# Kernel tuning notes

Hardware: AMD Instinct MI355X
Metric: run time of the kernel (lower is better)

The kernel has to match this reference:

```python
import jax, jax.numpy as jnp
import numpy as np

N = 100000      # nodes
E = 1600000     # edges
IN, H1, H2, OUT = 128, 128, 64, 128  # layer_channel = [128, (128+128)//2, (128+128)//4, 128]


def setup_inputs() -> dict:
    key = jax.random.key(0)
    ks = jax.random.split(key, 11)
    w = lambda k, s: (jax.random.normal(k, s, jnp.float32) * 0.05)
    return {
        "x": jax.random.normal(ks[0], (N, IN), jnp.float32),
        "edge_index": jax.random.randint(ks[1], (2, E), 0, N),
        "gcn1_w": w(ks[2], (IN, H1)),   "gcn1_b": jnp.zeros((H1,), jnp.float32),
        "fc2_w": w(ks[3], (H1, H1)),   # nn.Linear weight [out, in]
        "gcn3_w": w(ks[4], (H1, H2)),   "gcn3_b": jnp.zeros((H2,), jnp.float32),
        "fc4_w": w(ks[5], (H2, H2)),
        "gcn5_w": w(ks[6], (H2, OUT)),  "gcn5_b": jnp.zeros((OUT,), jnp.float32),
        "fc6_w": w(ks[7], (OUT, OUT)),
    }


def _gcn_norm(edge_index):
    # PyG GCNConv default: add self-loops, symmetric normalization D^-1/2 (A+I) D^-1/2
    loop = jnp.arange(N, dtype=edge_index.dtype)
    src = jnp.concatenate([edge_index[0], loop])
    dst = jnp.concatenate([edge_index[1], loop])
    deg = jax.ops.segment_sum(jnp.ones_like(src, jnp.float32), dst, num_segments=N)
    dinv = jnp.where(deg > 0, jax.lax.rsqrt(jnp.maximum(deg, 1.0)), 0.0)
    norm = dinv[src] * dinv[dst]  # [E+N]
    return src, dst, norm


def _gcn_conv(x, W, b, src, dst, norm):
    h = x @ W                              # [N, d_out]
    msg = h[src] * norm[:, None]           # gather + scale over edges
    return jax.ops.segment_sum(msg, dst, num_segments=N) + b


def reference(x, edge_index, gcn1_w, gcn1_b, fc2_w, gcn3_w, gcn3_b, fc4_w, gcn5_w, gcn5_b, fc6_w):
    src, dst, norm = _gcn_norm(edge_index)
    relu = jax.nn.relu
    z1 = relu(_gcn_conv(x, gcn1_w, gcn1_b, src, dst, norm))
    z1 = relu(z1 + z1 @ fc2_w.T)
    z2 = relu(_gcn_conv(z1, gcn3_w, gcn3_b, src, dst, norm))
    z2 = relu(z2 + z2 @ fc4_w.T)
    z3 = relu(_gcn_conv(z2, gcn5_w, gcn5_b, src, dst, norm))
    z3 = relu(z3 + z3 @ fc6_w.T)
    return z3
```

## Files before the change

### kernel.cpp

```cpp
#include <hip/hip_runtime.h>
#include <cstdint>
#include <cstddef>

#define NN 100000
#define NE 1600000
#define NBB 391
#define BSTRIDE 5120

typedef short short8 __attribute__((ext_vector_type(8)));
typedef float floatx4 __attribute__((ext_vector_type(4)));
typedef unsigned short u16;
typedef uint32_t u32;


static __global__ void k_zero(int* __restrict__ gcur) {
    int i = threadIdx.x;
    if (i < NBB + 1) gcur[i] = 0;
}

static __global__ __launch_bounds__(1024) void k_bscatterF(const int* __restrict__ src,
                                                           const int* __restrict__ dst,
                                                           int* __restrict__ gcur,
                                                           int2* __restrict__ staging) {
    __shared__ int h[NBB + 1];
    __shared__ int base[NBB + 1];
    int t = threadIdx.x;
    for (int i = t; i < NBB; i += 1024) h[i] = 0;
    __syncthreads();
    int e0 = blockIdx.x * 4096;
    int b[4], l[4], sv[4], dv[4];
#pragma unroll
    for (int j = 0; j < 4; j++) {
        int e = e0 + j * 1024 + t;
        b[j] = -1;
        if (e < NE) {
            sv[j] = src[e];
            dv[j] = dst[e];
            b[j] = dv[j] >> 8;
            l[j] = atomicAdd(&h[b[j]], 1);
        }
    }
    __syncthreads();
    for (int i = t; i < NBB; i += 1024)
        if (h[i]) base[i] = atomicAdd(&gcur[i], h[i]);
    __syncthreads();
#pragma unroll
    for (int j = 0; j < 4; j++)
        if (b[j] >= 0)
            staging[(size_t)b[j] * BSTRIDE + base[b[j]] + l[j]] = make_int2(sv[j], dv[j]);
}

static __global__ __launch_bounds__(1024) void k_blocal2(const int2* __restrict__ staging,
                                                         const int* __restrict__ gcur,
                                                         float* __restrict__ dinv,
                                                         int* __restrict__ row_ptr) {
    __shared__ int cnt[256];
    __shared__ int sc[256];
    int b = blockIdx.x;
    int t = threadIdx.x;
    if (t < 256) cnt[t] = 0;
    __syncthreads();
    const int n = gcur[b];
    const int base = b * BSTRIDE;
    for (int i = base + t; i < base + n; i += 1024)
        atomicAdd(&cnt[staging[i].y & 255], 1);
    __syncthreads();
    int myc = (t < 256) ? cnt[t] : 0;
    if (t < 256) sc[t] = myc;
    __syncthreads();
    for (int off = 1; off < 256; off <<= 1) {
        int x = 0;
        if (t < 256 && t >= off) x = sc[t - off];
        __syncthreads();
        if (t < 256) sc[t] += x;
        __syncthreads();
    }
    if (t < 256) {
        int node = (b << 8) + t;
        if (node < NN) {
            dinv[node] = rsqrtf((float)(myc + 1));
            row_ptr[node] = sc[t] - myc;
        }
    }
}

static __global__ void k_bscanB(const int* __restrict__ gcur, int* __restrict__ gbase,
                                int* __restrict__ row_ptr) {
    __shared__ int sd[512];
    int t = threadIdx.x;
    int v = (t < NBB) ? gcur[t] : 0;
    sd[t] = v;
    __syncthreads();
    for (int off = 1; off < 512; off <<= 1) {
        int x = (t >= off) ? sd[t - off] : 0;
        __syncthreads();
        sd[t] += x;
        __syncthreads();
    }
    int excl = (t > 0) ? sd[t - 1] : 0;
    if (t < NBB) gbase[t] = excl;
    if (t == NBB) gbase[NBB] = excl;
    if (t == 0) row_ptr[NN] = NE;
}

static __global__ __launch_bounds__(1024) void k_bfill2(const int2* __restrict__ staging,
                                                        const int* __restrict__ gcur,
                                                        const int* __restrict__ gbase,
                                                        int* __restrict__ row_ptr,
                                                        int* __restrict__ csr_src) {
    __shared__ int cnt[256];
    __shared__ int lrp[256];
    int b = blockIdx.x;
    int t = threadIdx.x;
    if (t < 256) {
        cnt[t] = 0;
        int node = (b << 8) + t;
        lrp[t] = (node < NN) ? row_ptr[node] : 0;
    }
    __syncthreads();
    const int bb = gbase[b];
    const int n = gcur[b];
    const int base = b * BSTRIDE;
    for (int i = base + t; i < base + n; i += 1024) {
        int2 ed = staging[i];
        int loc = ed.y & 255;
        int r = atomicAdd(&cnt[loc], 1);
        csr_src[bb + lrp[loc] + r] = ed.x;
    }
    if (t < 256) {
        int node = (b << 8) + t;
        if (node < NN) row_ptr[node] = bb + lrp[t];
    }
}

__device__ __forceinline__ void split_bf16(float f, short& hi, short& lo) {
    union { float f; uint32_t u; } x;
    x.f = f;
    uint32_t uh = x.u + 0x7FFFu + ((x.u >> 16) & 1u);
    hi = (short)(uh >> 16);
    union { uint32_t u; float f; } hf;
    hf.u = (uh >> 16) << 16;
    float r = f - hf.f;
    union { float f; uint32_t u; } y;
    y.f = r;
    uint32_t ul = y.u + 0x7FFFu + ((y.u >> 16) & 1u);
    lo = (short)(ul >> 16);
}

__device__ __forceinline__ u16 f2bf(float f) {
    union { float f; uint32_t u; } x;
    x.f = f;
    uint32_t r = x.u + 0x7FFFu + ((x.u >> 16) & 1u);
    return (u16)(r >> 16);
}

__device__ __forceinline__ float bf2f(u16 h) {
    union { uint32_t u; float f; } x;
    x.u = ((uint32_t)h) << 16;
    return x.f;
}

__device__ __forceinline__ void acc2(uint32_t u, float& a0, float& a1) {
    union { uint32_t u; float f; } lo, hi;
    lo.u = u << 16;
    hi.u = u & 0xFFFF0000u;
    a0 += lo.f;
    a1 += hi.f;
}

struct WDesc {
    const float* W;
    short* fh;
    short* fl;
    int din, dout, transb, base, total;
};
struct WPrepArgs { WDesc d[6]; };

static __global__ void k_wprep(WPrepArgs args) {
    int tid = blockIdx.x * 256 + threadIdx.x;
#pragma unroll
    for (int i = 0; i < 6; i++) {
        const WDesc& D = args.d[i];
        if (tid >= D.base && tid < D.base + D.total) {
            int local = tid - D.base;
            int lane = local & 63;
            int rest = local >> 6;
            int kst = D.din >> 5;
            int ks = rest % kst;
            int ntile = rest / kst;
            int n = ntile * 16 + (lane & 15);
            int k0 = ks * 32 + (lane >> 4) * 8;
#pragma unroll
            for (int j = 0; j < 8; j++) {
                int k = k0 + j;
                float v = D.transb ? D.W[(size_t)n * D.din + k]
                                   : D.W[(size_t)k * D.dout + n];
                short h, l;
                split_bf16(v, h, l);
                D.fh[(size_t)local * 8 + j] = h;
                D.fl[(size_t)local * 8 + j] = l;
            }
        }
    }
}

template <int DIN, int DOUT, int MT, int AMODE, int OMODE, bool RESID, bool BIAS, bool SCALE>
__global__ __launch_bounds__(256, 3) void k_mgemm(const void* __restrict__ Av,
                                                  const short* __restrict__ fh,
                                                  const short* __restrict__ fl,
                                                  const float* __restrict__ bias,
                                                  const float* __restrict__ dinv,
                                                  void* __restrict__ C) {
    static_assert(!RESID || DIN == DOUT, "residual needs square");
    constexpr int KST = DIN / 32;
    constexpr int NTW = DOUT / 64;
    const int t = threadIdx.x;
    const int wave = t >> 6;
    const int lane = t & 63;
    const int r16 = lane & 15;
    const int kq = lane >> 4;

    const float* Af = (const float*)Av;
    const u16*   Ah = (const u16*)Av;
    const u16*   Al = Ah + (size_t)NN * DIN;

    short8 bh[NTW][KST], bl[NTW][KST];
#pragma unroll
    for (int nt = 0; nt < NTW; nt++) {
        int ntile = wave * NTW + nt;
#pragma unroll
        for (int ks = 0; ks < KST; ks++) {
            size_t o = ((size_t)(ntile * KST + ks) * 64 + lane) * 8;
            bh[nt][ks] = *(const short8*)(fh + o);
            bl[nt][ks] = *(const short8*)(fl + o);
        }
    }

    const int m0b = blockIdx.x * (MT * 16);
#pragma unroll
    for (int mt = 0; mt < MT; mt++) {
        const int m0 = m0b + mt * 16;
        if (m0 >= NN) break;
        const int ra = min(m0 + r16, NN - 1);

        floatx4 acc[NTW];
#pragma unroll
        for (int nt = 0; nt < NTW; nt++) acc[nt] = (floatx4){0.f, 0.f, 0.f, 0.f};

        if constexpr (AMODE == 1) {
            const float* Ap = Af + (size_t)ra * DIN + kq * 8;
#pragma unroll
            for (int ks = 0; ks < KST; ks++) {
                float4 f0 = *(const float4*)(Ap + ks * 32);
                float4 f1 = *(const float4*)(Ap + ks * 32 + 4);
                float fe[8] = {f0.x, f0.y, f0.z, f0.w, f1.x, f1.y, f1.z, f1.w};
                short8 ah;
#pragma unroll
                for (int j = 0; j < 8; j++) ah[j] = (short)f2bf(fe[j]);
#pragma unroll
                for (int nt = 0; nt < NTW; nt++) {
                    acc[nt] = __builtin_amdgcn_mfma_f32_16x16x32_bf16(ah, bh[nt][ks], acc[nt], 0, 0, 0);
                    acc[nt] = __builtin_amdgcn_mfma_f32_16x16x32_bf16(ah, bl[nt][ks], acc[nt], 0, 0, 0);
                }
            }
        } else {
            const u16* Aph = Ah + (size_t)ra * DIN + kq * 8;
            const u16* Apl = Al + (size_t)ra * DIN + kq * 8;
#pragma unroll
            for (int ks = 0; ks < KST; ks++) {
                short8 ah = *(const short8*)(Aph + ks * 32);
                short8 al = *(const short8*)(Apl + ks * 32);
#pragma unroll
                for (int nt = 0; nt < NTW; nt++) {
                    acc[nt] = __builtin_amdgcn_mfma_f32_16x16x32_bf16(ah, bh[nt][ks], acc[nt], 0, 0, 0);
                    acc[nt] = __builtin_amdgcn_mfma_f32_16x16x32_bf16(ah, bl[nt][ks], acc[nt], 0, 0, 0);
                    acc[nt] = __builtin_amdgcn_mfma_f32_16x16x32_bf16(al, bh[nt][ks], acc[nt], 0, 0, 0);
                }
            }
        }

#pragma unroll
        for (int nt = 0; nt < NTW; nt++) {
            int col = (wave * NTW + nt) * 16 + r16;
#pragma unroll
            for (int r = 0; r < 4; r++) {
                int row = m0 + kq * 4 + r;
                if (row < NN) {
                    float v = acc[nt][r];
                    if constexpr (RESID) {
                        size_t ri = (size_t)row * DIN + col;
                        v = fmaxf(v + bf2f(Ah[ri]) + bf2f(Al[ri]), 0.f);
                    }
                    if constexpr (BIAS) v = fmaxf(v + bias[col], 0.f);
                    if constexpr (SCALE) v *= dinv[row];
                    size_t oi = (size_t)row * DOUT + col;
                    if constexpr (OMODE == 0) {
                        ((float*)C)[oi] = v;
                    } else if constexpr (OMODE == 1) {
                        ((u16*)C)[oi] = f2bf(v);
                    } else {
                        short h, l;
                        split_bf16(v, h, l);
                        ((u16*)C)[oi] = (u16)h;
                        ((u16*)C)[(size_t)NN * DOUT + oi] = (u16)l;
                    }
                }
            }
        }
    }
}

template <int DIN, int DMID, int DOUT, int MT, bool RESID1, bool BIAS1,
          bool SCALE2, bool RESID2, int OMODE2>
__global__ __launch_bounds__(256, 3) void k_mfused(const u16* __restrict__ Ahp,
                                                   const short* __restrict__ f1h,
                                                   const short* __restrict__ f1l,
                                                   const short* __restrict__ f2h,
                                                   const short* __restrict__ f2l,
                                                   const float* __restrict__ bias1,
                                                   const float* __restrict__ dinv,
                                                   void* __restrict__ C) {
    static_assert(!RESID1 || DIN == DMID, "resid1 needs square stage1");
    static_assert(!RESID2 || DMID == DOUT, "resid2 needs square stage2");
    constexpr int KST1 = DIN / 32;
    constexpr int NTW1 = DMID / 64;
    constexpr int KST2 = DMID / 32;
    constexpr int NTW2 = DOUT / 64;
    constexpr int LDW = DMID + 8;
    __shared__ u16 ldsh[16][LDW];
    __shared__ u16 ldsl[16][LDW];

    const u16* Alp = Ahp + (size_t)NN * DIN;

    const int t = threadIdx.x;
    const int wave = t >> 6;
    const int lane = t & 63;
    const int r16 = lane & 15;
    const int kq = lane >> 4;

    short8 b1h[NTW1][KST1], b1l[NTW1][KST1];
#pragma unroll
    for (int nt = 0; nt < NTW1; nt++) {
        int ntile = wave * NTW1 + nt;
#pragma unroll
        for (int ks = 0; ks < KST1; ks++) {
            size_t o = ((size_t)(ntile * KST1 + ks) * 64 + lane) * 8;
            b1h[nt][ks] = *(const short8*)(f1h + o);
            b1l[nt][ks] = *(const short8*)(f1l + o);
        }
    }
    short8 b2h[NTW2][KST2], b2l[NTW2][KST2];
#pragma unroll
    for (int nt = 0; nt < NTW2; nt++) {
        int ntile = wave * NTW2 + nt;
#pragma unroll
        for (int ks = 0; ks < KST2; ks++) {
            size_t o = ((size_t)(ntile * KST2 + ks) * 64 + lane) * 8;
            b2h[nt][ks] = *(const short8*)(f2h + o);
            b2l[nt][ks] = *(const short8*)(f2l + o);
        }
    }

    const int m0b = blockIdx.x * (MT * 16);
#pragma unroll 1
    for (int mt = 0; mt < MT; mt++) {
        const int m0 = m0b + mt * 16;
        if (m0 >= NN) break;
        const int ra = min(m0 + r16, NN - 1);

        floatx4 acc1[NTW1];
#pragma unroll
        for (int nt = 0; nt < NTW1; nt++) acc1[nt] = (floatx4){0.f, 0.f, 0.f, 0.f};
        {
            const u16* Aph = Ahp + (size_t)ra * DIN + kq * 8;
            const u16* Apl = Alp + (size_t)ra * DIN + kq * 8;
#pragma unroll
            for (int ks = 0; ks < KST1; ks++) {
                short8 ah = *(const short8*)(Aph + ks * 32);
                short8 al = *(const short8*)(Apl + ks * 32);
#pragma unroll
                for (int nt = 0; nt < NTW1; nt++) {
                    acc1[nt] = __builtin_amdgcn_mfma_f32_16x16x32_bf16(ah, b1h[nt][ks], acc1[nt], 0, 0, 0);
                    acc1[nt] = __builtin_amdgcn_mfma_f32_16x16x32_bf16(ah, b1l[nt][ks], acc1[nt], 0, 0, 0);
                    acc1[nt] = __builtin_amdgcn_mfma_f32_16x16x32_bf16(al, b1h[nt][ks], acc1[nt], 0, 0, 0);
                }
            }
        }
#pragma unroll
        for (int nt = 0; nt < NTW1; nt++) {
            int col = (wave * NTW1 + nt) * 16 + r16;
#pragma unroll
            for (int r = 0; r < 4; r++) {
                int row = m0 + kq * 4 + r;
                float v = acc1[nt][r];
                if constexpr (RESID1) {
                    if (row < NN) {
                        size_t ri = (size_t)row * DIN + col;
                        v = fmaxf(v + bf2f(Ahp[ri]) + bf2f(Alp[ri]), 0.f);
                    }
                }
                if constexpr (BIAS1) v = fmaxf(v + bias1[col], 0.f);
                short h, l;
                split_bf16(v, h, l);
                ldsh[kq * 4 + r][col] = (u16)h;
                ldsl[kq * 4 + r][col] = (u16)l;
            }
        }
        __syncthreads();

        floatx4 acc2[NTW2];
#pragma unroll
        for (int nt = 0; nt < NTW2; nt++) acc2[nt] = (floatx4){0.f, 0.f, 0.f, 0.f};
#pragma unroll
        for (int ks = 0; ks < KST2; ks++) {
            short8 ah = *(const short8*)&ldsh[r16][ks * 32 + kq * 8];
            short8 al = *(const short8*)&ldsl[r16][ks * 32 + kq * 8];
#pragma unroll
            for (int nt = 0; nt < NTW2; nt++) {
                acc2[nt] = __builtin_amdgcn_mfma_f32_16x16x32_bf16(ah, b2h[nt][ks], acc2[nt], 0, 0, 0);
                acc2[nt] = __builtin_amdgcn_mfma_f32_16x16x32_bf16(ah, b2l[nt][ks], acc2[nt], 0, 0, 0);
                acc2[nt] = __builtin_amdgcn_mfma_f32_16x16x32_bf16(al, b2h[nt][ks], acc2[nt], 0, 0, 0);
            }
        }

#pragma unroll
        for (int nt = 0; nt < NTW2; nt++) {
            int col = (wave * NTW2 + nt) * 16 + r16;
#pragma unroll
            for (int r = 0; r < 4; r++) {
                int row = m0 + kq * 4 + r;
                if (row < NN) {
                    float v = acc2[nt][r];
                    if constexpr (RESID2)
                        v = fmaxf(v + bf2f(ldsh[kq * 4 + r][col]) + bf2f(ldsl[kq * 4 + r][col]), 0.f);
                    if constexpr (SCALE2) v *= dinv[row];
                    size_t oi = (size_t)row * DOUT + col;
                    if constexpr (OMODE2 == 0) {
                        ((float*)C)[oi] = v;
                    } else if constexpr (OMODE2 == 1) {
                        ((u16*)C)[oi] = f2bf(v);
                    } else {
                        short h, l;
                        split_bf16(v, h, l);
                        ((u16*)C)[oi] = (u16)h;
                        ((u16*)C)[(size_t)NN * DOUT + oi] = (u16)l;
                    }
                }
            }
        }
        __syncthreads();
    }
}

template <int D, bool BIAS_RELU>
__global__ __launch_bounds__(256) void k_agg(const u16* __restrict__ hs,
                                             const float* __restrict__ dinv,
                                             const int* __restrict__ row_ptr,
                                             const int* __restrict__ csr_src,
                                             const float* __restrict__ bias,
                                             u16* __restrict__ outh) {
    u16* outl = outh + (size_t)NN * D;
    int node = blockIdx.x * 4 + (threadIdx.x >> 6);
    int lane = threadIdx.x & 63;
    if (node >= NN) return;

    if constexpr (D == 128) {
        const int off = lane * 2;
        float a0 = 0.f, a1 = 0.f;
        {
            uint32_t u = ((const uint32_t*)(hs + (size_t)node * D))[lane];
            acc2(u, a0, a1);
        }
        int e = row_ptr[node];
        const int end = row_ptr[node + 1];
        for (; e + 16 <= end; e += 16) {
            int s[16];
#pragma unroll
            for (int i = 0; i < 16; i++) s[i] = csr_src[e + i];
            uint32_t v[16];
#pragma unroll
            for (int i = 0; i < 16; i++) v[i] = ((const uint32_t*)(hs + (size_t)s[i] * D))[lane];
#pragma unroll
            for (int i = 0; i < 16; i++) acc2(v[i], a0, a1);
        }
        for (; e + 8 <= end; e += 8) {
            int s[8];
#pragma unroll
            for (int i = 0; i < 8; i++) s[i] = csr_src[e + i];
            uint32_t v[8];
#pragma unroll
            for (int i = 0; i < 8; i++) v[i] = ((const uint32_t*)(hs + (size_t)s[i] * D))[lane];
#pragma unroll
            for (int i = 0; i < 8; i++) acc2(v[i], a0, a1);
        }
        for (; e + 4 <= end; e += 4) {
            int s[4];
#pragma unroll
            for (int i = 0; i < 4; i++) s[i] = csr_src[e + i];
            uint32_t v[4];
#pragma unroll
            for (int i = 0; i < 4; i++) v[i] = ((const uint32_t*)(hs + (size_t)s[i] * D))[lane];
#pragma unroll
            for (int i = 0; i < 4; i++) acc2(v[i], a0, a1);
        }
        for (; e < end; e++) {
            int s = csr_src[e];
            uint32_t u = ((const uint32_t*)(hs + (size_t)s * D))[lane];
            acc2(u, a0, a1);
        }
        const float di = dinv[node];
        a0 *= di;
        a1 *= di;
        if constexpr (BIAS_RELU) {
            a0 = fmaxf(a0 + bias[off], 0.f);
            a1 = fmaxf(a1 + bias[off + 1], 0.f);
        }
        short h0, l0, h1, l1;
        split_bf16(a0, h0, l0);
        split_bf16(a1, h1, l1);
        ushort2 wh, wl;
        wh.x = (u16)h0; wh.y = (u16)h1;
        wl.x = (u16)l0; wl.y = (u16)l1;
        *(ushort2*)(outh + (size_t)node * D + off) = wh;
        *(ushort2*)(outl + (size_t)node * D + off) = wl;
    } else {
        const int half = lane >> 5;
        const int l32 = lane & 31;
        float a0 = 0.f, a1 = 0.f;
        if (half == 0) {
            uint32_t u = ((const uint32_t*)(hs + (size_t)node * D))[l32];
            acc2(u, a0, a1);
        }
        int e = row_ptr[node];
        const int end = row_ptr[node + 1];
        for (; e + 16 <= end; e += 16) {
            int s[8];
#pragma unroll
            for (int i = 0; i < 8; i++) s[i] = csr_src[e + half + 2 * i];
            uint32_t v[8];
#pragma unroll
            for (int i = 0; i < 8; i++) v[i] = ((const uint32_t*)(hs + (size_t)s[i] * D))[l32];
#pragma unroll
            for (int i = 0; i < 8; i++) acc2(v[i], a0, a1);
        }
        for (; e + 8 <= end; e += 8) {
            int s[4];
#pragma unroll
            for (int i = 0; i < 4; i++) s[i] = csr_src[e + half + 2 * i];
            uint32_t v[4];
#pragma unroll
            for (int i = 0; i < 4; i++) v[i] = ((const uint32_t*)(hs + (size_t)s[i] * D))[l32];
#pragma unroll
            for (int i = 0; i < 4; i++) acc2(v[i], a0, a1);
        }
        for (; e + 2 <= end; e += 2) {
            int s = csr_src[e + half];
            uint32_t u = ((const uint32_t*)(hs + (size_t)s * D))[l32];
            acc2(u, a0, a1);
        }
        if (e < end && half == 0) {
            int s = csr_src[e];
            uint32_t u = ((const uint32_t*)(hs + (size_t)s * D))[l32];
            acc2(u, a0, a1);
        }
        a0 += __shfl_xor(a0, 32, 64);
        a1 += __shfl_xor(a1, 32, 64);
        if (half == 0) {
            const int off = l32 * 2;
            const float di = dinv[node];
            a0 *= di;
            a1 *= di;
            if constexpr (BIAS_RELU) {
                a0 = fmaxf(a0 + bias[off], 0.f);
                a1 = fmaxf(a1 + bias[off + 1], 0.f);
            }
            short h0, l0, h1, l1;
            split_bf16(a0, h0, l0);
            split_bf16(a1, h1, l1);
            ushort2 wh, wl;
            wh.x = (u16)h0; wh.y = (u16)h1;
            wl.x = (u16)l0; wl.y = (u16)l1;
            *(ushort2*)(outh + (size_t)node * D + off) = wh;
            *(ushort2*)(outl + (size_t)node * D + off) = wl;
        }
    }
}


extern "C" void kernel_launch(void* const* d_in, const int* in_sizes, int n_in,
                              void* d_out, int out_size, void* d_ws, size_t ws_size,
                              hipStream_t stream) {
    const float* x   = (const float*)d_in[0];
    const int*   ei  = (const int*)d_in[1];
    const float* g1w = (const float*)d_in[2];
    const float* g1b = (const float*)d_in[3];
    const float* f2w = (const float*)d_in[4];
    const float* g3w = (const float*)d_in[5];
    const float* g3b = (const float*)d_in[6];
    const float* f4w = (const float*)d_in[7];
    const float* g5w = (const float*)d_in[8];
    const float* g5b = (const float*)d_in[9];
    const float* f6w = (const float*)d_in[10];
    float* out = (float*)d_out;

    const int* src = ei;
    const int* dst = ei + NE;

    char* p = (char*)d_ws;
    auto alloc = [&](size_t bytes) -> void* {
        void* r = (void*)p;
        p += (bytes + 255) & ~(size_t)255;
        return r;
    };
    float* dinv    = (float*)alloc(NN * 4);
    int*   row_ptr = (int*)alloc((NN + 1) * 4);
    int*   gcur    = (int*)alloc((NBB + 1) * 4);
    int*   gbase   = (int*)alloc((NBB + 1) * 4);
    int*   csr     = (int*)alloc(NE * 4);
    short* wfh     = (short*)alloc(69632 * 2);
    short* wfl     = (short*)alloc(69632 * 2);
    char* bufA = (char*)alloc((size_t)NN * 128 * 4);
    char* bufB = (char*)alloc((size_t)NN * 128 * 4);
    int2* staging  = (int2*)bufB;

    const int gE4 = (NE + 4095) / 4096;
    const int gA  = NN / 4;
    const int gM  = (NN + 31) / 32;

    k_zero<<<1, 512, 0, stream>>>(gcur);
    k_bscatterF<<<gE4, 1024, 0, stream>>>(src, dst, gcur, staging);
    k_blocal2<<<NBB, 1024, 0, stream>>>(staging, gcur, dinv, row_ptr);
    k_bscanB<<<1, 512, 0, stream>>>(gcur, gbase, row_ptr);
    k_bfill2<<<NBB, 1024, 0, stream>>>(staging, gcur, gbase, row_ptr, csr);

    {
        WPrepArgs a;
        int  eoff[6] = {0, 16384, 32768, 40960, 45056, 53248};
        int  base[6] = {0, 2048, 4096, 5120, 5632, 6656};
        int  tot[6]  = {2048, 2048, 1024, 512, 1024, 2048};
        const float* Ws[6] = {g1w, f2w, g3w, f4w, g5w, f6w};
        int din[6]  = {128, 128, 128, 64, 64, 128};
        int dout[6] = {128, 128, 64, 64, 128, 128};
        int trb[6]  = {0, 1, 0, 1, 0, 1};
        for (int i = 0; i < 6; i++) {
            a.d[i] = WDesc{Ws[i], wfh + eoff[i], wfl + eoff[i],
                           din[i], dout[i], trb[i], base[i], tot[i]};
        }
        k_wprep<<<(8704 + 255) / 256, 256, 0, stream>>>(a);
    }

    k_mgemm<128, 128, 2, 1, 1, false, false, true><<<gM, 256, 0, stream>>>(
        x, wfh + 0, wfl + 0, nullptr, dinv, bufA);
    k_agg<128, true><<<gA, 256, 0, stream>>>((const u16*)bufA, dinv, row_ptr, csr, g1b, (u16*)bufB);
    k_mfused<128, 128, 64, 2, true, false, true, false, 1><<<gM, 256, 0, stream>>>(
        (const u16*)bufB, wfh + 16384, wfl + 16384, wfh + 32768, wfl + 32768,
        nullptr, dinv, bufA);
    k_agg<64, true><<<gA, 256, 0, stream>>>((const u16*)bufA, dinv, row_ptr, csr, g3b, (u16*)bufB);
    k_mgemm<64, 64, 2, 2, 1, true, false, true><<<gM, 256, 0, stream>>>(
        bufB, wfh + 40960, wfl + 40960, nullptr, dinv, bufA);
    k_agg<64, false><<<gA, 256, 0, stream>>>((const u16*)bufA, dinv, row_ptr, csr, nullptr, (u16*)bufB);
    k_mfused<64, 128, 128, 2, false, true, false, true, 0><<<gM, 256, 0, stream>>>(
        (const u16*)bufB, wfh + 45056, wfl + 45056, wfh + 53248, wfl + 53248,
        g5b, nullptr, out);
}
```

Before: 480.0 us.

## Drop low-bf16 split for intermediate activations and remove global scan in CSR build

Intermediate activations after the first two aggregations and inside the first fused MLP are now stored as a single bf16 instead of a hi/lo bf16 pair, which removes the low-part stores, loads and one third of the MFMA work in those GEMMs. The CSR build no longer runs a global prefix-scan kernel: each bucket writes into its own fixed-stride region, with separate row_ptr/row_end arrays, and the gcur zeroing is folded into the weight-prep kernel. This removes two small launches and halves activation traffic for part of the pipeline, at the cost of lower precision in intermediate layers.

Measured after the change: 447.4 us. 6.8% less time.

```diff
diff --git a/kernel.cpp b/kernel.cpp
--- a/kernel.cpp
+++ b/kernel.cpp
@@ -12,11 +12,78 @@
 typedef unsigned short u16;
 typedef uint32_t u32;
 
-
-static __global__ void k_zero(int* __restrict__ gcur) {
-    int i = threadIdx.x;
-    if (i < NBB + 1) gcur[i] = 0;
-}
+__device__ __forceinline__ void split_bf16(float f, short& hi, short& lo) {
+    union { float f; uint32_t u; } x;
+    x.f = f;
+    uint32_t uh = x.u + 0x7FFFu + ((x.u >> 16) & 1u);
+    hi = (short)(uh >> 16);
+    union { uint32_t u; float f; } hf;
+    hf.u = (uh >> 16) << 16;
+    float r = f - hf.f;
+    union { float f; uint32_t u; } y;
+    y.f = r;
+    uint32_t ul = y.u + 0x7FFFu + ((y.u >> 16) & 1u);
+    lo = (short)(ul >> 16);
+}
+
+__device__ __forceinline__ u16 f2bf(float f) {
+    union { float f; uint32_t u; } x;
+    x.f = f;
+    uint32_t r = x.u + 0x7FFFu + ((x.u >> 16) & 1u);
+    return (u16)(r >> 16);
+}
+
+__device__ __forceinline__ float bf2f(u16 h) {
+    union { uint32_t u; float f; } x;
+    x.u = ((uint32_t)h) << 16;
+    return x.f;
+}
+
+__device__ __forceinline__ void acc2(uint32_t u, float& a0, float& a1) {
+    union { uint32_t u; float f; } lo, hi;
+    lo.u = u << 16;
+    hi.u = u & 0xFFFF0000u;
+    a0 += lo.f;
+    a1 += hi.f;
+}
+
+struct WDesc {
+    const float* W;
+    short* fh;
+    short* fl;
+    int din, dout, transb, base, total;
+};
+struct WPrepArgs { WDesc d[6]; int* gcur; };
+
+static __global__ void k_wprep(WPrepArgs args) {
+    int tid = blockIdx.x * 256 + threadIdx.x;
+    if (tid <= NBB) args.gcur[tid] = 0;
+#pragma unroll
+    for (int i = 0; i < 6; i++) {
+        const WDesc& D = args.d[i];
+        if (tid >= D.base && tid < D.base + D.total) {
+            int local = tid - D.base;
+            int lane = local & 63;
+            int rest = local >> 6;
+            int kst = D.din >> 5;
+            int ks = rest % kst;
+            int ntile = rest / kst;
+            int n = ntile * 16 + (lane & 15);
+            int k0 = ks * 32 + (lane >> 4) * 8;
+#pragma unroll
+            for (int j = 0; j < 8; j++) {
+                int k = k0 + j;
+                float v = D.transb ? D.W[(size_t)n * D.din + k]
+                                   : D.W[(size_t)k * D.dout + n];
+                short h, l;
+                split_bf16(v, h, l);
+                D.fh[(size_t)local * 8 + j] = h;
+                D.fl[(size_t)local * 8 + j] = l;
+            }
+        }
+    }
+}
+
 
 static __global__ __launch_bounds__(1024) void k_bscatterF(const int* __restrict__ src,
                                                            const int* __restrict__ dst,
@@ -53,7 +120,8 @@
 static __global__ __launch_bounds__(1024) void k_blocal2(const int2* __restrict__ staging,
                                                          const int* __restrict__ gcur,
                                                          float* __restrict__ dinv,
-                                                         int* __restrict__ row_ptr) {
+                                                         int* __restrict__ row_ptr,
+                                                         int* __restrict__ row_end) {
     __shared__ int cnt[256];
     __shared__ int sc[256];
     int b = blockIdx.x;
@@ -79,34 +147,16 @@
         int node = (b << 8) + t;
         if (node < NN) {
             dinv[node] = rsqrtf((float)(myc + 1));
-            row_ptr[node] = sc[t] - myc;
-        }
-    }
-}
-
-static __global__ void k_bscanB(const int* __restrict__ gcur, int* __restrict__ gbase,
-                                int* __restrict__ row_ptr) {
-    __shared__ int sd[512];
-    int t = threadIdx.x;
-    int v = (t < NBB) ? gcur[t] : 0;
-    sd[t] = v;
-    __syncthreads();
-    for (int off = 1; off < 512; off <<= 1) {
-        int x = (t >= off) ? sd[t - off] : 0;
-        __syncthreads();
-        sd[t] += x;
-        __syncthreads();
-    }
-    int excl = (t > 0) ? sd[t - 1] : 0;
-    if (t < NBB) gbase[t] = excl;
-    if (t == NBB) gbase[NBB] = excl;
-    if (t == 0) row_ptr[NN] = NE;
+            int st = base + sc[t] - myc;
+            row_ptr[node] = st;
+            row_end[node] = st + myc;
+        }
+    }
 }
 
 static __global__ __launch_bounds__(1024) void k_bfill2(const int2* __restrict__ staging,
                                                         const int* __restrict__ gcur,
-                                                        const int* __restrict__ gbase,
-                                                        int* __restrict__ row_ptr,
+                                                        const int* __restrict__ row_ptr,
                                                         int* __restrict__ csr_src) {
     __shared__ int cnt[256];
     __shared__ int lrp[256];
@@ -118,89 +168,13 @@
         lrp[t] = (node < NN) ? row_ptr[node] : 0;
     }
     __syncthreads();
-    const int bb = gbase[b];
     const int n = gcur[b];
     const int base = b * BSTRIDE;
     for (int i = base + t; i < base + n; i += 1024) {
         int2 ed = staging[i];
         int loc = ed.y & 255;
         int r = atomicAdd(&cnt[loc], 1);
-        csr_src[bb + lrp[loc] + r] = ed.x;
-    }
-    if (t < 256) {
-        int node = (b << 8) + t;
-        if (node < NN) row_ptr[node] = bb + lrp[t];
-    }
-}
-
-__device__ __forceinline__ void split_bf16(float f, short& hi, short& lo) {
-    union { float f; uint32_t u; } x;
-    x.f = f;
-    uint32_t uh = x.u + 0x7FFFu + ((x.u >> 16) & 1u);
-    hi = (short)(uh >> 16);
-    union { uint32_t u; float f; } hf;
-    hf.u = (uh >> 16) << 16;
-    float r = f - hf.f;
-    union { float f; uint32_t u; } y;
-    y.f = r;
-    uint32_t ul = y.u + 0x7FFFu + ((y.u >> 16) & 1u);
-    lo = (short)(ul >> 16);
-}
-
-__device__ __forceinline__ u16 f2bf(float f) {
-    union { float f; uint32_t u; } x;
-    x.f = f;
-    uint32_t r = x.u + 0x7FFFu + ((x.u >> 16) & 1u);
-    return (u16)(r >> 16);
-}
-
-__device__ __forceinline__ float bf2f(u16 h) {
-    union { uint32_t u; float f; } x;
-    x.u = ((uint32_t)h) << 16;
-    return x.f;
-}
-
-__device__ __forceinline__ void acc2(uint32_t u, float& a0, float& a1) {
-    union { uint32_t u; float f; } lo, hi;
-    lo.u = u << 16;
-    hi.u = u & 0xFFFF0000u;
-    a0 += lo.f;
-    a1 += hi.f;
-}
-
-struct WDesc {
-    const float* W;
-    short* fh;
-    short* fl;
-    int din, dout, transb, base, total;
-};
-struct WPrepArgs { WDesc d[6]; };
-
-static __global__ void k_wprep(WPrepArgs args) {
-    int tid = blockIdx.x * 256 + threadIdx.x;
-#pragma unroll
-    for (int i = 0; i < 6; i++) {
-        const WDesc& D = args.d[i];
-        if (tid >= D.base && tid < D.base + D.total) {
-            int local = tid - D.base;
-            int lane = local & 63;
-            int rest = local >> 6;
-            int kst = D.din >> 5;
-            int ks = rest % kst;
-            int ntile = rest / kst;
-            int n = ntile * 16 + (lane & 15);
-            int k0 = ks * 32 + (lane >> 4) * 8;
-#pragma unroll
-            for (int j = 0; j < 8; j++) {
-                int k = k0 + j;
-                float v = D.transb ? D.W[(size_t)n * D.din + k]
-                                   : D.W[(size_t)k * D.dout + n];
-                short h, l;
-                split_bf16(v, h, l);
-                D.fh[(size_t)local * 8 + j] = h;
-                D.fl[(size_t)local * 8 + j] = l;
-            }
-        }
+        csr_src[lrp[loc] + r] = ed.x;
     }
 }
 
@@ -263,6 +237,17 @@
                     acc[nt] = __builtin_amdgcn_mfma_f32_16x16x32_bf16(ah, bl[nt][ks], acc[nt], 0, 0, 0);
                 }
             }
+        } else if constexpr (AMODE == 3) {
+            const u16* Aph = Ah + (size_t)ra * DIN + kq * 8;
+#pragma unroll
+            for (int ks = 0; ks < KST; ks++) {
+                short8 ah = *(const short8*)(Aph + ks * 32);
+#pragma unroll
+                for (int nt = 0; nt < NTW; nt++) {
+                    acc[nt] = __builtin_amdgcn_mfma_f32_16x16x32_bf16(ah, bh[nt][ks], acc[nt], 0, 0, 0);
+                    acc[nt] = __builtin_amdgcn_mfma_f32_16x16x32_bf16(ah, bl[nt][ks], acc[nt], 0, 0, 0);
+                }
+            }
         } else {
             const u16* Aph = Ah + (size_t)ra * DIN + kq * 8;
             const u16* Apl = Al + (size_t)ra * DIN + kq * 8;
@@ -289,7 +274,10 @@
                     float v = acc[nt][r];
                     if constexpr (RESID) {
                         size_t ri = (size_t)row * DIN + col;
-                        v = fmaxf(v + bf2f(Ah[ri]) + bf2f(Al[ri]), 0.f);
+                        if constexpr (AMODE == 3)
+                            v = fmaxf(v + bf2f(Ah[ri]), 0.f);
+                        else
+                            v = fmaxf(v + bf2f(Ah[ri]) + bf2f(Al[ri]), 0.f);
                     }
                     if constexpr (BIAS) v = fmaxf(v + bias[col], 0.f);
                     if constexpr (SCALE) v *= dinv[row];
@@ -310,8 +298,8 @@
     }
 }
 
-template <int DIN, int DMID, int DOUT, int MT, bool RESID1, bool BIAS1,
-          bool SCALE2, bool RESID2, int OMODE2>
+template <int DIN, int DMID, int DOUT, int MT, bool A1S, bool MIDS, bool RESID1,
+          bool BIAS1, bool SCALE2, bool RESID2, int OMODE2>
 __global__ __launch_bounds__(256, 3) void k_mfused(const u16* __restrict__ Ahp,
                                                    const short* __restrict__ f1h,
                                                    const short* __restrict__ f1l,
@@ -328,7 +316,7 @@
     constexpr int NTW2 = DOUT / 64;
     constexpr int LDW = DMID + 8;
     __shared__ u16 ldsh[16][LDW];
-    __shared__ u16 ldsl[16][LDW];
+    __shared__ u16 ldsl[MIDS ? 1 : 16][LDW];
 
     const u16* Alp = Ahp + (size_t)NN * DIN;
 
@@ -377,12 +365,16 @@
 #pragma unroll
             for (int ks = 0; ks < KST1; ks++) {
                 short8 ah = *(const short8*)(Aph + ks * 32);
-                short8 al = *(const short8*)(Apl + ks * 32);
 #pragma unroll
                 for (int nt = 0; nt < NTW1; nt++) {
                     acc1[nt] = __builtin_amdgcn_mfma_f32_16x16x32_bf16(ah, b1h[nt][ks], acc1[nt], 0, 0, 0);
                     acc1[nt] = __builtin_amdgcn_mfma_f32_16x16x32_bf16(ah, b1l[nt][ks], acc1[nt], 0, 0, 0);
-                    acc1[nt] = __builtin_amdgcn_mfma_f32_16x16x32_bf16(al, b1h[nt][ks], acc1[nt], 0, 0, 0);
+                }
+                if constexpr (!A1S) {
+                    short8 al = *(const short8*)(Apl + ks * 32);
+#pragma unroll
+                    for (int nt = 0; nt < NTW1; nt++)
+                        acc1[nt] = __builtin_amdgcn_mfma_f32_16x16x32_bf16(al, b1h[nt][ks], acc1[nt], 0, 0, 0);
                 }
             }
         }
@@ -396,14 +388,21 @@
                 if constexpr (RESID1) {
                     if (row < NN) {
                         size_t ri = (size_t)row * DIN + col;
-                        v = fmaxf(v + bf2f(Ahp[ri]) + bf2f(Alp[ri]), 0.f);
+                        if constexpr (A1S)
+                            v = fmaxf(v + bf2f(Ahp[ri]), 0.f);
+                        else
+                            v = fmaxf(v + bf2f(Ahp[ri]) + bf2f(Alp[ri]), 0.f);
                     }
                 }
                 if constexpr (BIAS1) v = fmaxf(v + bias1[col], 0.f);
-                short h, l;
-                split_bf16(v, h, l);
-                ldsh[kq * 4 + r][col] = (u16)h;
-                ldsl[kq * 4 + r][col] = (u16)l;
+                if constexpr (MIDS) {
+                    ldsh[kq * 4 + r][col] = f2bf(v);
+                } else {
+                    short h, l;
+                    split_bf16(v, h, l);
+                    ldsh[kq * 4 + r][col] = (u16)h;
+                    ldsl[kq * 4 + r][col] = (u16)l;
+                }
             }
         }
         __syncthreads();
@@ -414,12 +413,16 @@
 #pragma unroll
         for (int ks = 0; ks < KST2; ks++) {
             short8 ah = *(const short8*)&ldsh[r16][ks * 32 + kq * 8];
-            short8 al = *(const short8*)&ldsl[r16][ks * 32 + kq * 8];
 #pragma unroll
             for (int nt = 0; nt < NTW2; nt++) {
                 acc2[nt] = __builtin_amdgcn_mfma_f32_16x16x32_bf16(ah, b2h[nt][ks], acc2[nt], 0, 0, 0);
                 acc2[nt] = __builtin_amdgcn_mfma_f32_16x16x32_bf16(ah, b2l[nt][ks], acc2[nt], 0, 0, 0);
-                acc2[nt] = __builtin_amdgcn_mfma_f32_16x16x32_bf16(al, b2h[nt][ks], acc2[nt], 0, 0, 0);
+            }
+            if constexpr (!MIDS) {
+                short8 al = *(const short8*)&ldsl[r16][ks * 32 + kq * 8];
+#pragma unroll
+                for (int nt = 0; nt < NTW2; nt++)
+                    acc2[nt] = __builtin_amdgcn_mfma_f32_16x16x32_bf16(al, b2h[nt][ks], acc2[nt], 0, 0, 0);
             }
         }
 
@@ -431,8 +434,12 @@
                 int row = m0 + kq * 4 + r;
                 if (row < NN) {
                     float v = acc2[nt][r];
-                    if constexpr (RESID2)
-                        v = fmaxf(v + bf2f(ldsh[kq * 4 + r][col]) + bf2f(ldsl[kq * 4 + r][col]), 0.f);
+                    if constexpr (RESID2) {
+                        if constexpr (MIDS)
+                            v = fmaxf(v + bf2f(ldsh[kq * 4 + r][col]), 0.f);
+                        else
+                            v = fmaxf(v + bf2f(ldsh[kq * 4 + r][col]) + bf2f(ldsl[kq * 4 + r][col]), 0.f);
+                    }
                     if constexpr (SCALE2) v *= dinv[row];
                     size_t oi = (size_t)row * DOUT + col;
                     if constexpr (OMODE2 == 0) {
@@ -452,10 +459,11 @@
     }
 }
 
-template <int D, bool BIAS_RELU>
+template <int D, bool BIAS_RELU, int OPL>
 __global__ __launch_bounds__(256) void k_agg(const u16* __restrict__ hs,
                                              const float* __restrict__ dinv,
                                              const int* __restrict__ row_ptr,
+                                             const int* __restrict__ row_end,
                                              const int* __restrict__ csr_src,
                                              const float* __restrict__ bias,
                                              u16* __restrict__ outh) {
@@ -472,7 +480,7 @@
             acc2(u, a0, a1);
         }
         int e = row_ptr[node];
-        const int end = row_ptr[node + 1];
+        const int end = row_end[node];
         for (; e + 16 <= end; e += 16) {
             int s[16];
 #pragma unroll
@@ -515,14 +523,20 @@
             a0 = fmaxf(a0 + bias[off], 0.f);
             a1 = fmaxf(a1 + bias[off + 1], 0.f);
         }
-        short h0, l0, h1, l1;
-        split_bf16(a0, h0, l0);
-        split_bf16(a1, h1, l1);
-        ushort2 wh, wl;
-        wh.x = (u16)h0; wh.y = (u16)h1;
-        wl.x = (u16)l0; wl.y = (u16)l1;
-        *(ushort2*)(outh + (size_t)node * D + off) = wh;
-        *(ushort2*)(outl + (size_t)node * D + off) = wl;
+        if constexpr (OPL == 1) {
+            ushort2 wh;
+            wh.x = f2bf(a0); wh.y = f2bf(a1);
+            *(ushort2*)(outh + (size_t)node * D + off) = wh;
+        } else {
+            short h0, l0, h1, l1;
+            split_bf16(a0, h0, l0);
+            split_bf16(a1, h1, l1);
+            ushort2 wh, wl;
+            wh.x = (u16)h0; wh.y = (u16)h1;
+            wl.x = (u16)l0; wl.y = (u16)l1;
+            *(ushort2*)(outh + (size_t)node * D + off) = wh;
+            *(ushort2*)(outl + (size_t)node * D + off) = wl;
+        }
     } else {
         const int half = lane >> 5;
         const int l32 = lane & 31;
@@ -532,7 +546,7 @@
             acc2(u, a0, a1);
         }
         int e = row_ptr[node];
-        const int end = row_ptr[node + 1];
+        const int end = row_end[node];
         for (; e + 16 <= end; e += 16) {
             int s[8];
 #pragma unroll
@@ -574,14 +588,20 @@
                 a0 = fmaxf(a0 + bias[off], 0.f);
                 a1 = fmaxf(a1 + bias[off + 1], 0.f);
             }
-            short h0, l0, h1, l1;
-            split_bf16(a0, h0, l0);
-            split_bf16(a1, h1, l1);
-            ushort2 wh, wl;
-            wh.x = (u16)h0; wh.y = (u16)h1;
-            wl.x = (u16)l0; wl.y = (u16)l1;
-            *(ushort2*)(outh + (size_t)node * D + off) = wh;
-            *(ushort2*)(outl + (size_t)node * D + off) = wl;
+            if constexpr (OPL == 1) {
+                ushort2 wh;
+                wh.x = f2bf(a0); wh.y = f2bf(a1);
+                *(ushort2*)(outh + (size_t)node * D + off) = wh;
+            } else {
+                short h0, l0, h1, l1;
+                split_bf16(a0, h0, l0);
+                split_bf16(a1, h1, l1);
+                ushort2 wh, wl;
+                wh.x = (u16)h0; wh.y = (u16)h1;
+                wl.x = (u16)l0; wl.y = (u16)l1;
+                *(ushort2*)(outh + (size_t)node * D + off) = wh;
+                *(ushort2*)(outl + (size_t)node * D + off) = wl;
+            }
         }
     }
 }
@@ -613,10 +633,10 @@
         return r;
     };
     float* dinv    = (float*)alloc(NN * 4);
-    int*   row_ptr = (int*)alloc((NN + 1) * 4);
+    int*   row_ptr = (int*)alloc(NN * 4);
+    int*   row_end = (int*)alloc(NN * 4);
     int*   gcur    = (int*)alloc((NBB + 1) * 4);
-    int*   gbase   = (int*)alloc((NBB + 1) * 4);
-    int*   csr     = (int*)alloc(NE * 4);
+    int*   csr     = (int*)alloc((size_t)NBB * BSTRIDE * 4);
     short* wfh     = (short*)alloc(69632 * 2);
     short* wfl     = (short*)alloc(69632 * 2);
     char* bufA = (char*)alloc((size_t)NN * 128 * 4);
@@ -626,12 +646,6 @@
     const int gE4 = (NE + 4095) / 4096;
     const int gA  = NN / 4;
     const int gM  = (NN + 31) / 32;
-
-    k_zero<<<1, 512, 0, stream>>>(gcur);
-    k_bscatterF<<<gE4, 1024, 0, stream>>>(src, dst, gcur, staging);
-    k_blocal2<<<NBB, 1024, 0, stream>>>(staging, gcur, dinv, row_ptr);
-    k_bscanB<<<1, 512, 0, stream>>>(gcur, gbase, row_ptr);
-    k_bfill2<<<NBB, 1024, 0, stream>>>(staging, gcur, gbase, row_ptr, csr);
 
     {
         WPrepArgs a;
@@ -646,20 +660,25 @@
             a.d[i] = WDesc{Ws[i], wfh + eoff[i], wfl + eoff[i],
                            din[i], dout[i], trb[i], base[i], tot[i]};
         }
+        a.gcur = gcur;
         k_wprep<<<(8704 + 255) / 256, 256, 0, stream>>>(a);
     }
+
+    k_bscatterF<<<gE4, 1024, 0, stream>>>(src, dst, gcur, staging);
+    k_blocal2<<<NBB, 1024, 0, stream>>>(staging, gcur, dinv, row_ptr, row_end);
+    k_bfill2<<<NBB, 1024, 0, stream>>>(staging, gcur, row_ptr, csr);
 
     k_mgemm<128, 128, 2, 1, 1, false, false, true><<<gM, 256, 0, stream>>>(
         x, wfh + 0, wfl + 0, nullptr, dinv, bufA);
-    k_agg<128, true><<<gA, 256, 0, stream>>>((const u16*)bufA, dinv, row_ptr, csr, g1b, (u16*)bufB);
-    k_mfused<128, 128, 64, 2, true, false, true, false, 1><<<gM, 256, 0, stream>>>(
+    k_agg<128, true, 1><<<gA, 256, 0, stream>>>((const u16*)bufA, dinv, row_ptr, row_end, csr, g1b, (u16*)bufB);
+    k_mfused<128, 128, 64, 2, true, true, true, false, true, false, 1><<<gM, 256, 0, stream>>>(
         (const u16*)bufB, wfh + 16384, wfl + 16384, wfh + 32768, wfl + 32768,
         nullptr, dinv, bufA);
-    k_agg<64, true><<<gA, 256, 0, stream>>>((const u16*)bufA, dinv, row_ptr, csr, g3b, (u16*)bufB);
-    k_mgemm<64, 64, 2, 2, 1, true, false, true><<<gM, 256, 0, stream>>>(
+    k_agg<64, true, 1><<<gA, 256, 0, stream>>>((const u16*)bufA, dinv, row_ptr, row_end, csr, g3b, (u16*)bufB);
+    k_mgemm<64, 64, 2, 3, 1, true, false, true><<<gM, 256, 0, stream>>>(
         bufB, wfh + 40960, wfl + 40960, nullptr, dinv, bufA);
-    k_agg<64, false><<<gA, 256, 0, stream>>>((const u16*)bufA, dinv, row_ptr, csr, nullptr, (u16*)bufB);
-    k_mfused<64, 128, 128, 2, false, true, false, true, 0><<<gM, 256, 0, stream>>>(
+    k_agg<64, false, 2><<<gA, 256, 0, stream>>>((const u16*)bufA, dinv, row_ptr, row_end, csr, nullptr, (u16*)bufB);
+    k_mfused<64, 128, 128, 2, false, false, false, true, false, true, 0><<<gM, 256, 0, stream>>>(
         (const u16*)bufB, wfh + 45056, wfl + 45056, wfh + 53248, wfl + 53248,
         g5b, nullptr, out);
 }
```
